# Kernel tuning notes

Hardware: AMD Instinct MI355X
Metric: run time of the kernel (lower is better)

The kernel has to match this reference:

```python
import jax, jax.numpy as jnp
import numpy as np

B, C, HW, SCALE = 8, 512, 64, 8
M = C // SCALE  # Q/K channel dim
EPS = 1e-6


def setup_inputs() -> dict:
    key = jax.random.key(0)
    ks = jax.random.split(key, 8)
    s = 0.02
    return {
        "x": jax.random.normal(ks[0], (B, C, HW, HW), dtype=jnp.float32),
        "wq": jax.random.normal(ks[1], (M, C), dtype=jnp.float32) * s,
        "bq": jax.random.normal(ks[2], (M,), dtype=jnp.float32) * s,
        "wk": jax.random.normal(ks[3], (M, C), dtype=jnp.float32) * s,
        "bk": jax.random.normal(ks[4], (M,), dtype=jnp.float32) * s,
        "wv": jax.random.normal(ks[5], (C, C), dtype=jnp.float32) * s,
        "bv": jax.random.normal(ks[6], (C,), dtype=jnp.float32) * s,
        "gamma": jax.random.normal(ks[7], (1,), dtype=jnp.float32),
    }


def reference(x, wq, bq, wk, bk, wv, bv, gamma):
    b, c, w, h = x.shape
    n = w * h
    xf = x.reshape(b, c, n)  # [B,C,N]
    # 1x1 convs == channel GEMMs
    Q = jnp.einsum('bcn,mc->bmn', xf, wq) + bq[None, :, None]  # [B,M,N]
    K = jnp.einsum('bcn,mc->bmn', xf, wk) + bk[None, :, None]  # [B,M,N]
    V = jnp.einsum('bcn,oc->bon', xf, wv) + bv[None, :, None]  # [B,C,N]
    # pooling gate: global max + global avg over spatial dims -> [B,C,1]
    gate = (jnp.max(xf, axis=-1) + jnp.mean(xf, axis=-1))[:, :, None]
    V = gate * V
    Qf = jax.nn.softplus(Q).transpose(0, 2, 1)  # [B,N,M]
    Kf = jax.nn.softplus(K)                      # [B,M,N]
    KV = jnp.einsum('bmn,bcn->bmc', Kf, V)       # [B,M,C]
    norm = 1.0 / jnp.einsum('bnm,bm->bn', Qf, jnp.sum(Kf, axis=-1) + EPS)  # [B,N]
    wval = jnp.einsum('bnm,bmc,bn->bcn', Qf, KV, norm)  # [B,C,N]
    wval = wval.reshape(b, c, h, w)
    return x + gamma * wval
```

## Files before the change

### kernel.cpp

```cpp
#include <hip/hip_runtime.h>
#include <math.h>

#define Bb 8
#define Cc 512
#define Nn 4096
#define Mm 64
#define OC 640
#define EPSf 1e-6f

typedef unsigned short ushort_t;
typedef unsigned int uint_t;
typedef __attribute__((ext_vector_type(8))) short short8;
typedef __attribute__((ext_vector_type(4))) float f32x4;

constexpr size_t OFF_GATE = 0;
constexpr size_t OFF_BCAT = OFF_GATE + (size_t)Bb * Cc;
constexpr size_t OFF_GPM  = OFF_BCAT + (size_t)OC;
constexpr size_t OFF_GPS  = OFF_GPM + (size_t)64 * Bb * Cc;
constexpr size_t OFF_WBF  = OFF_GPS + (size_t)64 * Bb * Cc;
constexpr size_t OFF_XT   = OFF_WBF + (size_t)OC * Cc / 2;
constexpr size_t OFF_QBF  = OFF_XT + (size_t)Bb * Nn * Cc / 2;
constexpr size_t OFF_KBF  = OFF_QBF + (size_t)Bb * Mm * Nn / 2;
constexpr size_t OFF_VBF  = OFF_KBF + (size_t)Bb * Mm * Nn / 2;
constexpr size_t OFF_KVBF = OFF_VBF + (size_t)Bb * Cc * Nn / 2;
constexpr size_t OFF_KSUM = OFF_KVBF + (size_t)Bb * Cc * Mm / 2;
constexpr size_t OFF_NORM = OFF_KSUM + (size_t)Bb * Mm;
constexpr size_t OFF_QT   = OFF_NORM + (size_t)Bb * Nn;

__device__ __forceinline__ float softplus_f(float v) {
    return fmaxf(v, 0.f) + __logf(1.f + __expf(-fabsf(v)));
}
__device__ __forceinline__ ushort_t f2bf(float f) {
    uint_t u = __float_as_uint(f);
    uint_t r = (u + 0x7fffu + ((u >> 16) & 1u)) >> 16;
    return (ushort_t)r;
}
__device__ __forceinline__ float bf2f(ushort_t h) {
    return __uint_as_float(((uint_t)h) << 16);
}
__device__ __forceinline__ void gload_lds16(const void* g, void* l) {
    __builtin_amdgcn_global_load_lds(
        (const __attribute__((address_space(1))) unsigned int*)g,
        (__attribute__((address_space(3))) unsigned int*)l, 16, 0, 0);
}
#define BARRIER()   asm volatile("s_barrier" ::: "memory")
#define WAIT_VM(N)  asm volatile("s_waitcnt vmcnt(" #N ")" ::: "memory")

__global__ void wconv_k(const float* __restrict__ wq, const float* __restrict__ bq,
                        const float* __restrict__ wk, const float* __restrict__ bk,
                        const float* __restrict__ wv, const float* __restrict__ bv,
                        ushort_t* __restrict__ wbf, float* __restrict__ bcat) {
    int i = blockIdx.x * 256 + threadIdx.x;
    if (i < OC * Cc) {
        int o = i / Cc, c = i % Cc;
        float v;
        if (o < Mm)            v = wq[o * Cc + c];
        else if (o < 2 * Mm)   v = wk[(o - Mm) * Cc + c];
        else                   v = wv[(o - 2 * Mm) * Cc + c];
        wbf[i] = f2bf(v);
    }
    if (i < OC) {
        float v;
        if (i < Mm)            v = bq[i];
        else if (i < 2 * Mm)   v = bk[i - Mm];
        else                   v = bv[i - 2 * Mm];
        bcat[i] = v;
    }
}

__global__ __launch_bounds__(256) void xtrans_k(const float* __restrict__ x, ushort_t* __restrict__ xT,
                                                float* __restrict__ gpm, float* __restrict__ gps) {
    const int nb = blockIdx.x * 64;
    const int cb = blockIdx.y * 64;
    const int b  = blockIdx.z;
    __shared__ float Xt[64][65];
    __shared__ float pmx[4][64], psm[4][64];
    const int t = threadIdx.x;
    #pragma unroll
    for (int r = 0; r < 16; r++) {
        int cl = (t >> 6) + r * 4;
        int nl = t & 63;
        Xt[cl][nl] = x[((size_t)b * Cc + cb + cl) * Nn + nb + nl];
    }
    __syncthreads();
    #pragma unroll
    for (int r = 0; r < 8; r++) {
        int nl = (t >> 5) + r * 8;
        int c0 = (t & 31) * 2;
        uint_t pk = (uint_t)f2bf(Xt[c0][nl]) | ((uint_t)f2bf(Xt[c0 + 1][nl]) << 16);
        *(uint_t*)(xT + ((size_t)b * Nn + nb + nl) * Cc + cb + c0) = pk;
    }
    {
        int cl = t & 63, q = t >> 6;
        float mx = -3.4e38f, sm = 0.f;
        #pragma unroll
        for (int j = 0; j < 16; j++) {
            float v = Xt[cl][q * 16 + j];
            mx = fmaxf(mx, v); sm += v;
        }
        pmx[q][cl] = mx; psm[q][cl] = sm;
    }
    __syncthreads();
    if (t < 64) {
        float mx = fmaxf(fmaxf(pmx[0][t], pmx[1][t]), fmaxf(pmx[2][t], pmx[3][t]));
        float sm = psm[0][t] + psm[1][t] + psm[2][t] + psm[3][t];
        size_t idx = (size_t)blockIdx.x * (Bb * Cc) + (size_t)b * Cc + cb + t;
        gpm[idx] = mx;
        gps[idx] = sm;
    }
}

__global__ void gatered_k(const float* __restrict__ gpm, const float* __restrict__ gps,
                          float* __restrict__ gate) {
    int bc = blockIdx.x;
    int l = threadIdx.x;
    float mx = gpm[(size_t)l * (Bb * Cc) + bc];
    float sm = gps[(size_t)l * (Bb * Cc) + bc];
    #pragma unroll
    for (int off = 32; off; off >>= 1) {
        mx = fmaxf(mx, __shfl_xor(mx, off));
        sm += __shfl_xor(sm, off);
    }
    if (l == 0) gate[bc] = mx + sm * (1.f / Nn);
}

__global__ __launch_bounds__(256, 4) void qkv_mfma_k(const ushort_t* __restrict__ wbf,
                                                     const ushort_t* __restrict__ xT,
                                                     const float* __restrict__ bcat,
                                                     ushort_t* __restrict__ Qbf,
                                                     ushort_t* __restrict__ Kbf,
                                                     ushort_t* __restrict__ Vbf) {
    const int nb  = blockIdx.x * 128;
    const int oty = blockIdx.y;
    const int b   = blockIdx.z;
    __shared__ ushort_t At[3][2048];
    __shared__ ushort_t Bt[3][4096];
    const int tid  = threadIdx.x;
    const int w    = tid >> 6;
    const int lane = tid & 63;
    const int wr   = w >> 1, wc = w & 1;
    const int hi   = lane >> 4, lo = lane & 15;
    const int rA   = tid >> 2;
    const int kc   = (((tid & 3) ^ ((tid >> 3) & 3)) * 8);
    const int sx   = (hi ^ ((lo >> 1) & 3)) * 8;
    const ushort_t* xb = xT + ((size_t)b * Nn + nb) * Cc;
    const ushort_t* wb = wbf + (size_t)oty * 64 * Cc;

    f32x4 acc[2][4] = {};

    auto stage = [&](int buf, int kb) {
        gload_lds16(wb + (size_t)rA * Cc + kb + kc,        &At[buf][w * 512]);
        gload_lds16(xb + (size_t)rA * Cc + kb + kc,        &Bt[buf][w * 512]);
        gload_lds16(xb + (size_t)(64 + rA) * Cc + kb + kc, &Bt[buf][2048 + w * 512]);
    };
    auto compute = [&](int buf) {
        short8 a[2], bfr[4];
        #pragma unroll
        for (int mi = 0; mi < 2; mi++)
            a[mi] = *(const short8*)(&At[buf][(wr * 32 + mi * 16 + lo) * 32 + sx]);
        #pragma unroll
        for (int ni = 0; ni < 4; ni++)
            bfr[ni] = *(const short8*)(&Bt[buf][(wc * 64 + ni * 16 + lo) * 32 + sx]);
        #pragma unroll
        for (int mi = 0; mi < 2; mi++)
            #pragma unroll
            for (int ni = 0; ni < 4; ni++)
                acc[mi][ni] = __builtin_amdgcn_mfma_f32_16x16x32_bf16(a[mi], bfr[ni], acc[mi][ni], 0, 0, 0);
    };

    stage(0, 0);
    stage(1, 32);
    #pragma unroll
    for (int t = 0; t < 16; ++t) {
        if (t < 15) { WAIT_VM(3); } else { WAIT_VM(0); }
        BARRIER();
        if (t + 2 < 16) stage((t + 2) % 3, (t + 2) * 32);
        compute(t % 3);
    }

    ushort_t* dst0;
    if (oty == 0)      dst0 = Qbf + (size_t)b * Mm * Nn;
    else if (oty == 1) dst0 = Kbf + (size_t)b * Mm * Nn;
    else               dst0 = Vbf + ((size_t)b * Cc + (oty - 2) * 64) * Nn;

    if (oty < 2) {
        #pragma unroll
        for (int mi = 0; mi < 2; mi++)
            #pragma unroll
            for (int r = 0; r < 4; r++) {
                const int ol = wr * 32 + mi * 16 + hi * 4 + r;
                const float bias = bcat[oty * 64 + ol];
                ushort_t* dst = dst0 + (size_t)ol * Nn + nb + wc * 64;
                #pragma unroll
                for (int ni = 0; ni < 4; ni++)
                    dst[ni * 16 + lo] = f2bf(softplus_f(acc[mi][ni][r] + bias));
            }
    } else {
        #pragma unroll
        for (int mi = 0; mi < 2; mi++)
            #pragma unroll
            for (int r = 0; r < 4; r++) {
                const int ol = wr * 32 + mi * 16 + hi * 4 + r;
                const float bias = bcat[oty * 64 + ol];
                ushort_t* dst = dst0 + (size_t)ol * Nn + nb + wc * 64;
                #pragma unroll
                for (int ni = 0; ni < 4; ni++)
                    dst[ni * 16 + lo] = f2bf(acc[mi][ni][r] + bias);
            }
    }
}

__global__ __launch_bounds__(256) void ksum_k(const ushort_t* __restrict__ Kbf, float* __restrict__ Ksum) {
    int bm = blockIdx.x;
    const ushort_t* row = Kbf + (size_t)bm * Nn;
    int t = threadIdx.x;
    float sm = 0.f;
    for (int i = t * 8; i < Nn; i += 2048) {
        short8 v = *(const short8*)(row + i);
        #pragma unroll
        for (int j = 0; j < 8; j++) sm += bf2f((ushort_t)v[j]);
    }
    #pragma unroll
    for (int off = 32; off; off >>= 1) sm += __shfl_xor(sm, off);
    __shared__ float ssm[4];
    if ((t & 63) == 0) ssm[t >> 6] = sm;
    __syncthreads();
    if (t == 0) Ksum[bm] = ssm[0] + ssm[1] + ssm[2] + ssm[3];
}

__global__ __launch_bounds__(256, 3) void kv_mfma_k(const ushort_t* __restrict__ Kbf,
                                                    const ushort_t* __restrict__ Vbf,
                                                    float* __restrict__ KVpart) {
    const int cb = blockIdx.x * 128;
    const int split = blockIdx.y;
    const int b = blockIdx.z;
    __shared__ ushort_t Vt[2][4096];
    __shared__ ushort_t Kt[2][2048];
    const int tid = threadIdx.x;
    const int w = tid >> 6, lane = tid & 63;
    const int hi = lane >> 4, lo = lane & 15;
    const int rwl = lane >> 2;
    const int kc  = (((lane & 3) ^ ((lane >> 3) & 3)) * 8);
    const int sx  = (hi ^ ((lo >> 1) & 3)) * 8;
    const ushort_t* Vb = Vbf + (size_t)b * Cc * Nn;
    const ushort_t* Kb = Kbf + (size_t)b * Mm * Nn;
    const int nbase = split * 512;

    f32x4 acc[2][4] = {};

    auto stage = [&](int buf, int n0) {
        #pragma unroll
        for (int li = 0; li < 2; li++) {
            const int rw = (w * 2 + li) * 16 + rwl;
            gload_lds16(Vb + (size_t)(cb + rw) * Nn + n0 + kc, &Vt[buf][(w * 2 + li) * 512]);
        }
        gload_lds16(Kb + (size_t)(w * 16 + rwl) * Nn + n0 + kc, &Kt[buf][w * 512]);
    };
    auto compute = [&](int buf) {
        short8 a[2], bv[4];
        #pragma unroll
        for (int mi = 0; mi < 2; mi++)
            a[mi] = *(const short8*)(&Vt[buf][(w * 32 + mi * 16 + lo) * 32 + sx]);
        #pragma unroll
        for (int ni = 0; ni < 4; ni++)
            bv[ni] = *(const short8*)(&Kt[buf][(ni * 16 + lo) * 32 + sx]);
        #pragma unroll
        for (int mi = 0; mi < 2; mi++)
            #pragma unroll
            for (int ni = 0; ni < 4; ni++)
                acc[mi][ni] = __builtin_amdgcn_mfma_f32_16x16x32_bf16(a[mi], bv[ni], acc[mi][ni], 0, 0, 0);
    };

    stage(0, nbase);
    #pragma unroll
    for (int t = 0; t < 16; ++t) {
        if (t < 15) {
            stage((t + 1) & 1, nbase + (t + 1) * 32);
            WAIT_VM(3);
        } else {
            WAIT_VM(0);
        }
        BARRIER();
        compute(t & 1);
        BARRIER();
    }

    float* dst = KVpart + (size_t)(split * Bb + b) * Cc * Mm;
    #pragma unroll
    for (int mi = 0; mi < 2; mi++)
        #pragma unroll
        for (int r = 0; r < 4; r++) {
            const int c = cb + w * 32 + mi * 16 + hi * 4 + r;
            #pragma unroll
            for (int ni = 0; ni < 4; ni++)
                dst[(size_t)c * Mm + ni * 16 + lo] = acc[mi][ni][r];
        }
}

__global__ __launch_bounds__(256) void kvred_k(const float* __restrict__ KVpart,
                                               const float* __restrict__ gate,
                                               ushort_t* __restrict__ KVbf) {
    int i = blockIdx.x * 256 + threadIdx.x;
    const f32x4* p = (const f32x4*)KVpart;
    f32x4 s = p[i];
    #pragma unroll
    for (int sp = 1; sp < 8; sp++) s += p[(size_t)sp * 65536 + i];
    int idx4 = i * 4;
    int b = idx4 >> 15;
    int c = (idx4 >> 6) & (Cc - 1);
    float g = gate[b * Cc + c];
    uint2 pk;
    pk.x = (uint_t)f2bf(s[0] * g) | ((uint_t)f2bf(s[1] * g) << 16);
    pk.y = (uint_t)f2bf(s[2] * g) | ((uint_t)f2bf(s[3] * g) << 16);
    *(uint2*)(KVbf + (size_t)i * 4) = pk;
}

__global__ __launch_bounds__(256) void qtransnorm_k(const ushort_t* __restrict__ Qbf,
                                                    const float* __restrict__ Ksum,
                                                    ushort_t* __restrict__ QT,
                                                    float* __restrict__ normb) {
    const int n0 = blockIdx.x * 64;
    const int b  = blockIdx.y;
    __shared__ float Qs[64][65];
    __shared__ float ks[64];
    __shared__ float ps[4][64];
    const int t = threadIdx.x;
    if (t < 64) ks[t] = Ksum[b * Mm + t] + EPSf;
    {
        int m = t >> 2, q = t & 3;
        const ushort_t* src = Qbf + ((size_t)b * Mm + m) * Nn + n0 + q * 16;
        short8 v0 = *(const short8*)(src);
        short8 v1 = *(const short8*)(src + 8);
        #pragma unroll
        for (int j = 0; j < 8; j++) {
            Qs[m][q * 16 + j]     = bf2f((ushort_t)v0[j]);
            Qs[m][q * 16 + 8 + j] = bf2f((ushort_t)v1[j]);
        }
    }
    __syncthreads();
    {
        int n = t & 63, ch = t >> 6;
        float s = 0.f;
        #pragma unroll
        for (int j = 0; j < 16; j++) s += Qs[ch * 16 + j][n] * ks[ch * 16 + j];
        ps[ch][n] = s;
    }
    __syncthreads();
    if (t < 64) normb[(size_t)b * Nn + n0 + t] = 1.f / (ps[0][t] + ps[1][t] + ps[2][t] + ps[3][t]);
    #pragma unroll
    for (int i = 0; i < 2; i++) {
        int u = t + i * 256;
        int n = u >> 3, j = u & 7;
        short8 v;
        #pragma unroll
        for (int jj = 0; jj < 8; jj++) v[jj] = (short)f2bf(Qs[j * 8 + jj][n]);
        *(short8*)(QT + ((size_t)b * Nn + n0 + n) * Mm + j * 8) = v;
    }
}

__global__ __launch_bounds__(256, 2) void final_mfma_k(const float* __restrict__ x,
                                                       const ushort_t* __restrict__ QT,
                                                       const ushort_t* __restrict__ KVbf,
                                                       const float* __restrict__ normb,
                                                       const float* __restrict__ gamma,
                                                       float* __restrict__ out) {
    const int nb = blockIdx.x * 128;
    const int cb = blockIdx.y * 128;
    const int b  = blockIdx.z;
    __shared__ ushort_t Qs[128 * 64];
    __shared__ ushort_t Ks[128 * 64];
    const int tid  = threadIdx.x;
    const int w    = tid >> 6;
    const int lane = tid & 63;
    const int wr   = w >> 1, wc = w & 1;
    const int hi   = lane >> 4, lo = lane & 15;
    const int lr   = lane >> 3;
    const int swz  = (((lane & 7) ^ (lr & 7)) * 8);
    const ushort_t* Qb = QT + (size_t)b * Nn * Mm;
    const ushort_t* Kb = KVbf + (size_t)b * Cc * Mm;

    #pragma unroll
    for (int p = 0; p < 4; p++) {
        const int rb = p * 32 + w * 8;
        gload_lds16(Qb + (size_t)(nb + rb + lr) * Mm + swz, &Qs[rb * 64]);
        gload_lds16(Kb + (size_t)(cb + rb + lr) * Mm + swz, &Ks[rb * 64]);
    }
    __syncthreads();

    f32x4 acc[4][4] = {};
    #pragma unroll
    for (int kk = 0; kk < 2; kk++) {
        short8 a[4], bfr[4];
        #pragma unroll
        for (int mi = 0; mi < 4; mi++) {
            const int row = wr * 64 + mi * 16 + lo;
            a[mi] = *(const short8*)(&Qs[row * 64 + (((kk * 4 + hi) ^ (lo & 7)) * 8)]);
        }
        #pragma unroll
        for (int ni = 0; ni < 4; ni++) {
            const int row = wc * 64 + ni * 16 + lo;
            bfr[ni] = *(const short8*)(&Ks[row * 64 + (((kk * 4 + hi) ^ (lo & 7)) * 8)]);
        }
        #pragma unroll
        for (int mi = 0; mi < 4; mi++)
            #pragma unroll
            for (int ni = 0; ni < 4; ni++)
                acc[mi][ni] = __builtin_amdgcn_mfma_f32_16x16x32_bf16(a[mi], bfr[ni], acc[mi][ni], 0, 0, 0);
    }

    const float g = gamma[0];
    #pragma unroll
    for (int mi = 0; mi < 4; mi++) {
        const int n0 = nb + wr * 64 + mi * 16 + hi * 4;
        float4 nrm = *(const float4*)(normb + (size_t)b * Nn + n0);
        #pragma unroll
        for (int ni = 0; ni < 4; ni++) {
            const int c = cb + wc * 64 + ni * 16 + lo;
            size_t idx = ((size_t)b * Cc + c) * Nn + n0;
            float4 xv = *(const float4*)(x + idx);
            float4 o;
            o.x = xv.x + g * nrm.x * acc[mi][ni][0];
            o.y = xv.y + g * nrm.y * acc[mi][ni][1];
            o.z = xv.z + g * nrm.z * acc[mi][ni][2];
            o.w = xv.w + g * nrm.w * acc[mi][ni][3];
            *(float4*)(out + idx) = o;
        }
    }
}

extern "C" void kernel_launch(void* const* d_in, const int* in_sizes, int n_in,
                              void* d_out, int out_size, void* d_ws, size_t ws_size,
                              hipStream_t stream) {
    const float* x     = (const float*)d_in[0];
    const float* wq    = (const float*)d_in[1];
    const float* bq    = (const float*)d_in[2];
    const float* wk    = (const float*)d_in[3];
    const float* bk    = (const float*)d_in[4];
    const float* wv    = (const float*)d_in[5];
    const float* bv    = (const float*)d_in[6];
    const float* gamma = (const float*)d_in[7];
    float* out = (float*)d_out;
    float* ws  = (float*)d_ws;

    float*    gate   = ws + OFF_GATE;
    float*    bcat   = ws + OFF_BCAT;
    float*    gpm    = ws + OFF_GPM;
    float*    gps    = ws + OFF_GPS;
    ushort_t* wbf    = (ushort_t*)(ws + OFF_WBF);
    ushort_t* xT     = (ushort_t*)(ws + OFF_XT);
    float*    KVpart = ws + OFF_XT;
    ushort_t* Qbf    = (ushort_t*)(ws + OFF_QBF);
    ushort_t* Kbf    = (ushort_t*)(ws + OFF_KBF);
    ushort_t* Vbf    = (ushort_t*)(ws + OFF_VBF);
    ushort_t* KVbf   = (ushort_t*)(ws + OFF_KVBF);
    float*    Ksum   = ws + OFF_KSUM;
    float*    normb  = ws + OFF_NORM;
    ushort_t* QT     = (ushort_t*)(ws + OFF_QT);

    wconv_k<<<(OC * Cc + 255) / 256, 256, 0, stream>>>(wq, bq, wk, bk, wv, bv, wbf, bcat);
    xtrans_k<<<dim3(Nn / 64, Cc / 64, Bb), 256, 0, stream>>>(x, xT, gpm, gps);
    gatered_k<<<Bb * Cc, 64, 0, stream>>>(gpm, gps, gate);
    qkv_mfma_k<<<dim3(Nn / 128, OC / 64, Bb), 256, 0, stream>>>(wbf, xT, bcat, Qbf, Kbf, Vbf);
    ksum_k<<<Bb * Mm, 256, 0, stream>>>(Kbf, Ksum);
    kv_mfma_k<<<dim3(Cc / 128, 8, Bb), 256, 0, stream>>>(Kbf, Vbf, KVpart);
    kvred_k<<<(Bb * Cc * Mm / 4) / 256, 256, 0, stream>>>(KVpart, gate, KVbf);
    qtransnorm_k<<<dim3(Nn / 64, Bb), 256, 0, stream>>>(Qbf, Ksum, QT, normb);
    final_mfma_k<<<dim3(Nn / 128, Cc / 128, Bb), 256, 0, stream>>>(x, QT, KVbf, normb, gamma, out);
}
```

Baseline: 116.2 us.

## Fuse K row-sum into QKV epilogue and vectorize x loads in transpose

Removes the separate ksum kernel by having the QKV GEMM epilogue reduce softplus(K) across lanes and atomically add into a zeroed Ksum buffer. The x transpose kernel now loads float4 instead of scalar floats, the GEMM raises wave priority around its MFMA block, and the final kernel's launch bound moves from 2 to 4 blocks. Risks include fp32 atomic ordering nondeterminism, an extra memset launch, and register pressure from the higher occupancy target. The Ksum is now summed from fp32 softplus values rather than their bf16-rounded copies.

```diff
diff --git a/kernel.cpp b/kernel.cpp
--- a/kernel.cpp
+++ b/kernel.cpp
@@ -77,10 +77,14 @@
     __shared__ float pmx[4][64], psm[4][64];
     const int t = threadIdx.x;
     #pragma unroll
-    for (int r = 0; r < 16; r++) {
-        int cl = (t >> 6) + r * 4;
-        int nl = t & 63;
-        Xt[cl][nl] = x[((size_t)b * Cc + cb + cl) * Nn + nb + nl];
+    for (int it = 0; it < 4; it++) {
+        int cl = it * 16 + (t >> 4);
+        int n0 = (t & 15) * 4;
+        float4 v = *(const float4*)(x + ((size_t)b * Cc + cb + cl) * Nn + nb + n0);
+        Xt[cl][n0 + 0] = v.x;
+        Xt[cl][n0 + 1] = v.y;
+        Xt[cl][n0 + 2] = v.z;
+        Xt[cl][n0 + 3] = v.w;
     }
     __syncthreads();
     #pragma unroll
@@ -129,7 +133,8 @@
                                                      const float* __restrict__ bcat,
                                                      ushort_t* __restrict__ Qbf,
                                                      ushort_t* __restrict__ Kbf,
-                                                     ushort_t* __restrict__ Vbf) {
+                                                     ushort_t* __restrict__ Vbf,
+                                                     float* __restrict__ Ksum) {
     const int nb  = blockIdx.x * 128;
     const int oty = blockIdx.y;
     const int b   = blockIdx.z;
@@ -161,11 +166,13 @@
         #pragma unroll
         for (int ni = 0; ni < 4; ni++)
             bfr[ni] = *(const short8*)(&Bt[buf][(wc * 64 + ni * 16 + lo) * 32 + sx]);
+        __builtin_amdgcn_s_setprio(1);
         #pragma unroll
         for (int mi = 0; mi < 2; mi++)
             #pragma unroll
             for (int ni = 0; ni < 4; ni++)
                 acc[mi][ni] = __builtin_amdgcn_mfma_f32_16x16x32_bf16(a[mi], bfr[ni], acc[mi][ni], 0, 0, 0);
+        __builtin_amdgcn_s_setprio(0);
     };
 
     stage(0, 0);
@@ -178,54 +185,51 @@
         compute(t % 3);
     }
 
-    ushort_t* dst0;
-    if (oty == 0)      dst0 = Qbf + (size_t)b * Mm * Nn;
-    else if (oty == 1) dst0 = Kbf + (size_t)b * Mm * Nn;
-    else               dst0 = Vbf + ((size_t)b * Cc + (oty - 2) * 64) * Nn;
-
-    if (oty < 2) {
+    if (oty == 0) {
         #pragma unroll
         for (int mi = 0; mi < 2; mi++)
             #pragma unroll
             for (int r = 0; r < 4; r++) {
                 const int ol = wr * 32 + mi * 16 + hi * 4 + r;
-                const float bias = bcat[oty * 64 + ol];
-                ushort_t* dst = dst0 + (size_t)ol * Nn + nb + wc * 64;
+                const float bias = bcat[ol];
+                ushort_t* dst = Qbf + ((size_t)b * Mm + ol) * Nn + nb + wc * 64;
                 #pragma unroll
                 for (int ni = 0; ni < 4; ni++)
                     dst[ni * 16 + lo] = f2bf(softplus_f(acc[mi][ni][r] + bias));
             }
+    } else if (oty == 1) {
+        #pragma unroll
+        for (int mi = 0; mi < 2; mi++)
+            #pragma unroll
+            for (int r = 0; r < 4; r++) {
+                const int ol = wr * 32 + mi * 16 + hi * 4 + r;
+                const float bias = bcat[Mm + ol];
+                ushort_t* dst = Kbf + ((size_t)b * Mm + ol) * Nn + nb + wc * 64;
+                float s = 0.f;
+                #pragma unroll
+                for (int ni = 0; ni < 4; ni++) {
+                    float sp = softplus_f(acc[mi][ni][r] + bias);
+                    dst[ni * 16 + lo] = f2bf(sp);
+                    s += sp;
+                }
+                s += __shfl_xor(s, 1); s += __shfl_xor(s, 2);
+                s += __shfl_xor(s, 4); s += __shfl_xor(s, 8);
+                if (lo == 0) atomicAdd(&Ksum[b * Mm + ol], s);
+            }
     } else {
+        const int cbase = (oty - 2) * 64;
         #pragma unroll
         for (int mi = 0; mi < 2; mi++)
             #pragma unroll
             for (int r = 0; r < 4; r++) {
                 const int ol = wr * 32 + mi * 16 + hi * 4 + r;
                 const float bias = bcat[oty * 64 + ol];
-                ushort_t* dst = dst0 + (size_t)ol * Nn + nb + wc * 64;
+                ushort_t* dst = Vbf + ((size_t)b * Cc + cbase + ol) * Nn + nb + wc * 64;
                 #pragma unroll
                 for (int ni = 0; ni < 4; ni++)
                     dst[ni * 16 + lo] = f2bf(acc[mi][ni][r] + bias);
             }
     }
-}
-
-__global__ __launch_bounds__(256) void ksum_k(const ushort_t* __restrict__ Kbf, float* __restrict__ Ksum) {
-    int bm = blockIdx.x;
-    const ushort_t* row = Kbf + (size_t)bm * Nn;
-    int t = threadIdx.x;
-    float sm = 0.f;
-    for (int i = t * 8; i < Nn; i += 2048) {
-        short8 v = *(const short8*)(row + i);
-        #pragma unroll
-        for (int j = 0; j < 8; j++) sm += bf2f((ushort_t)v[j]);
-    }
-    #pragma unroll
-    for (int off = 32; off; off >>= 1) sm += __shfl_xor(sm, off);
-    __shared__ float ssm[4];
-    if ((t & 63) == 0) ssm[t >> 6] = sm;
-    __syncthreads();
-    if (t == 0) Ksum[bm] = ssm[0] + ssm[1] + ssm[2] + ssm[3];
 }
 
 __global__ __launch_bounds__(256, 3) void kv_mfma_k(const ushort_t* __restrict__ Kbf,
@@ -358,7 +362,7 @@
     }
 }
 
-__global__ __launch_bounds__(256, 2) void final_mfma_k(const float* __restrict__ x,
+__global__ __launch_bounds__(256, 4) void final_mfma_k(const float* __restrict__ x,
                                                        const ushort_t* __restrict__ QT,
                                                        const ushort_t* __restrict__ KVbf,
                                                        const float* __restrict__ normb,
@@ -460,8 +464,8 @@
     wconv_k<<<(OC * Cc + 255) / 256, 256, 0, stream>>>(wq, bq, wk, bk, wv, bv, wbf, bcat);
     xtrans_k<<<dim3(Nn / 64, Cc / 64, Bb), 256, 0, stream>>>(x, xT, gpm, gps);
     gatered_k<<<Bb * Cc, 64, 0, stream>>>(gpm, gps, gate);
-    qkv_mfma_k<<<dim3(Nn / 128, OC / 64, Bb), 256, 0, stream>>>(wbf, xT, bcat, Qbf, Kbf, Vbf);
-    ksum_k<<<Bb * Mm, 256, 0, stream>>>(Kbf, Ksum);
+    hipMemsetAsync(Ksum, 0, (size_t)Bb * Mm * sizeof(float), stream);
+    qkv_mfma_k<<<dim3(Nn / 128, OC / 64, Bb), 256, 0, stream>>>(wbf, xT, bcat, Qbf, Kbf, Vbf, Ksum);
     kv_mfma_k<<<dim3(Cc / 128, 8, Bb), 256, 0, stream>>>(Kbf, Vbf, KVpart);
     kvred_k<<<(Bb * Cc * Mm / 4) / 256, 256, 0, stream>>>(KVpart, gate, KVbf);
     qtransnorm_k<<<dim3(Nn / 64, Bb), 256, 0, stream>>>(Qbf, Ksum, QT, normb);
```

Result: slower. 119.5 us (+2.8%).
